# Kernel optimization log

Hardware: AMD Instinct MI355X
Metric: run time of the kernel (lower is better)

## Reference

```python
import jax, jax.numpy as jnp
import numpy as np

D_MODEL = 512
N_HEADS = 8
D_K = D_MODEL // N_HEADS


def setup_inputs() -> dict:
    key = jax.random.key(0)
    kq, kk, kv = jax.random.split(key, 3)
    shape = (4, 2048, D_MODEL)
    return {
        "Q": jax.random.normal(kq, shape, dtype=jnp.float32),
        "K": jax.random.normal(kk, shape, dtype=jnp.float32),
        "V": jax.random.normal(kv, shape, dtype=jnp.float32),
    }


def reference(Q, K, V):
    B, S, _ = Q.shape
    # [B, S, H, Dk] -> [B, H, S, Dk]
    q = Q.reshape(B, S, N_HEADS, D_K).transpose(0, 2, 1, 3)
    k = K.reshape(B, S, N_HEADS, D_K).transpose(0, 2, 1, 3)
    v = V.reshape(B, S, N_HEADS, D_K).transpose(0, 2, 1, 3)
    scale = 1.0 / (D_K ** 0.5)
    # [B, H, S, S] scores (faithful to original: full matrix materialized)
    scores = jnp.einsum("bhqd,bhkd->bhqk", q, k) * scale
    attn = jax.nn.softmax(scores, axis=-1)
    out = jnp.einsum("bhqk,bhkd->bhqd", attn, v)
    # [B, H, S, Dk] -> [B, S, D_MODEL]
    return out.transpose(0, 2, 1, 3).reshape(B, S, D_MODEL)
```

## Files before the change

kernel.cpp:

```cpp
#include <hip/hip_runtime.h>
#include <hip/hip_bf16.h>

#define SEQ    2048
#define DMODEL 512
#define NH     8
#define QBLK   128
#define KVB    64
#define NT     (SEQ / KVB)

#if __has_builtin(__builtin_amdgcn_exp2f)
#define EXPFN(x) __builtin_amdgcn_exp2f(x)
#define QSCALE 0.18033688011112042f
#else
#define EXPFN(x) __expf(x)
#define QSCALE 0.125f
#endif
#define THR 8.0f

typedef __attribute__((ext_vector_type(8)))  short bf16x8;
typedef __attribute__((ext_vector_type(16))) float f32x16;
typedef __attribute__((ext_vector_type(2)))  int   i32x2;

#define MFMA32(A, B, C) __builtin_amdgcn_mfma_f32_32x32x16_bf16(A, B, C, 0, 0, 0)

__device__ __forceinline__ unsigned short f2bf(float f) {
  union { float f; unsigned u; } x; x.f = f;
  return (unsigned short)((x.u + 0x7FFFu + ((x.u >> 16) & 1u)) >> 16);
}

__device__ __forceinline__ int cvtpk(float lo, float hi) {
  int r;
  asm("v_cvt_pk_bf16_f32 %0, %1, %2" : "=v"(r) : "v"(lo), "v"(hi));
  return r;
}

__device__ __forceinline__ i32x2 plswap(int a, int b) {
#if __has_builtin(__builtin_amdgcn_permlane32_swap)
  return __builtin_amdgcn_permlane32_swap(a, b, false, false);
#else
  int a2 = __shfl_xor(a, 32), b2 = __shfl_xor(b, 32);
  int hi = (threadIdx.x >> 5) & 1;
  i32x2 r; r.x = hi ? b2 : a; r.y = hi ? b : a2; return r;
#endif
}

__device__ __forceinline__ void gload16(const void* g, void* l) {
  __builtin_amdgcn_global_load_lds(
      (const __attribute__((address_space(1))) void*)g,
      (__attribute__((address_space(3))) void*)l, 16, 0, 0);
}


__global__ void prep_kv(const float* __restrict__ K, const float* __restrict__ V,
                        unsigned short* __restrict__ kb, unsigned short* __restrict__ vb) {
  if (blockIdx.x < 2048) {
    int gid = blockIdx.x * 256 + threadIdx.x;
    int g  = gid & 7;
    int s  = (gid >> 3) & (SEQ - 1);
    int bh = gid >> 14;
    int b = bh >> 3, h = bh & 7;
    const float* src = K + ((size_t)(b * SEQ + s) * DMODEL) + h * 64 + (g << 3);
    float4 a = ((const float4*)src)[0];
    float4 c = ((const float4*)src)[1];
    bf16x8 w;
    w[0] = (short)f2bf(a.x); w[1] = (short)f2bf(a.y);
    w[2] = (short)f2bf(a.z); w[3] = (short)f2bf(a.w);
    w[4] = (short)f2bf(c.x); w[5] = (short)f2bf(c.y);
    w[6] = (short)f2bf(c.z); w[7] = (short)f2bf(c.w);
    int r = s & 63;
    int slot = ((((r >> 5) << 3) + g) ^ (r & 15));
    unsigned short* dst = kb + ((size_t)bh * SEQ + (s & ~63)) * 64
                             + ((r & 31) << 7) + (slot << 3);
    *(bf16x8*)dst = w;
  } else {
    int bt = blockIdx.x - 2048;
    int bh = bt >> 5, tile = bt & 31;
    int b = bh >> 3, h = bh & 7;
    int t  = threadIdx.x;
    int d  = t & 63;
    int kg = t >> 6;
    const float* src = V + ((size_t)(b * SEQ + tile * 64 + kg * 16) * DMODEL) + h * 64 + d;
    float v[16];
#pragma unroll
    for (int j = 0; j < 16; ++j) v[j] = src[(size_t)j * DMODEL];
    bf16x8 lo, hi;
#pragma unroll
    for (int j = 0; j < 8; ++j) { lo[j] = (short)f2bf(v[j]); hi[j] = (short)f2bf(v[8 + j]); }
    unsigned short* base = vb + ((size_t)bt << 12);
    int g0 = kg << 1, g1 = (kg << 1) | 1;
    int rb = (((d >> 5) << 3));
    int s0 = ((rb + g0) ^ (d & 15));
    int s1 = ((rb + g1) ^ (d & 15));
    unsigned short* row = base + ((d & 31) << 7);
    *(bf16x8*)(row + (s0 << 3)) = lo;
    *(bf16x8*)(row + (s1 << 3)) = hi;
  }
}

__global__ __launch_bounds__(256, 2)
void fa_fwd(const float* __restrict__ Q, const unsigned short* __restrict__ Kb,
            const unsigned short* __restrict__ Vb, float* __restrict__ O) {
  __shared__ unsigned short kt[4][KVB * 64];
  __shared__ unsigned short vt[4][64 * KVB];

  const int tid = threadIdx.x;
  const int wv  = tid >> 6;
  const int ln  = tid & 63;
  const int l31 = ln & 31;
  const int hi  = ln >> 5;

  const int orig = blockIdx.x;
  const int wgid = (orig & 7) * 64 + (orig >> 3);
  const int bh = wgid >> 4;
  const int qt = wgid & 15;
  const int b = bh >> 3, h = bh & 7;

  const float* Qh = Q + (size_t)b * SEQ * DMODEL + (size_t)h * 64;
  float*       Oh = O + (size_t)b * SEQ * DMODEL + (size_t)h * 64;
  const unsigned short* Kh = Kb + (size_t)bh * SEQ * 64;
  const unsigned short* Vh = Vb + (size_t)bh * SEQ * 64;

  const int q = qt * QBLK + wv * 32 + l31;

  bf16x8 qf[4];
  {
    const float* qp = Qh + (size_t)q * DMODEL + (hi << 3);
#pragma unroll
    for (int t = 0; t < 4; ++t) {
      float4 a = *(const float4*)(qp + 16 * t);
      float4 c = *(const float4*)(qp + 16 * t + 4);
      bf16x8 w;
      w[0] = (short)f2bf(a.x * QSCALE); w[1] = (short)f2bf(a.y * QSCALE);
      w[2] = (short)f2bf(a.z * QSCALE); w[3] = (short)f2bf(a.w * QSCALE);
      w[4] = (short)f2bf(c.x * QSCALE); w[5] = (short)f2bf(c.y * QSCALE);
      w[6] = (short)f2bf(c.z * QSCALE); w[7] = (short)f2bf(c.w * QSCALE);
      qf[t] = w;
    }
  }

  const int rowb = l31 << 7;
  int ca[4], cb[4];
#pragma unroll
  for (int t = 0; t < 4; ++t) {
    int g = 2 * t + hi;
    ca[t] = rowb + (((g)     ^ (l31 & 15)) << 3);
    cb[t] = rowb + (((8 + g) ^ (l31 & 15)) << 3);
  }

  f32x16 o0 = {}, o1 = {};
  f32x16 sA0, sA1, sB0, sB1;
  float m = -__builtin_inff();
  float l = 0.f;

#define STAGE(T, B)                                                        \
  do {                                                                     \
    const char* gk = (const char*)(Kh + (size_t)(T) * KVB * 64);           \
    const char* gv = (const char*)(Vh + (size_t)(T) * KVB * 64);           \
    char* lk = (char*)&kt[(B)][0];                                         \
    char* lv = (char*)&vt[(B)][0];                                         \
    gload16(gk + (((wv)     * 64 + ln) << 4), lk + ((wv)     << 10));      \
    gload16(gk + (((wv + 4) * 64 + ln) << 4), lk + ((wv + 4) << 10));      \
    gload16(gv + (((wv)     * 64 + ln) << 4), lv + ((wv)     << 10));      \
    gload16(gv + (((wv + 4) * 64 + ln) << 4), lv + ((wv + 4) << 10));      \
  } while (0)

  auto qk = [&](const unsigned short* ktb, f32x16& t0, f32x16& t1) {
    f32x16 u0 = {}, u1 = {};
#pragma unroll
    for (int ks = 0; ks < 4; ++ks) {
      bf16x8 k0 = *(const bf16x8*)&ktb[ca[ks]];
      bf16x8 k1 = *(const bf16x8*)&ktb[cb[ks]];
      __builtin_amdgcn_s_setprio(1);
      u0 = MFMA32(k0, qf[ks], u0);
      u1 = MFMA32(k1, qf[ks], u1);
      __builtin_amdgcn_s_setprio(0);
    }
    t0 = u0; t1 = u1;
  };

  auto smpv = [&](f32x16& s0, f32x16& s1, const unsigned short* vtb) {
    float pm = fmaxf(s0[0], s0[1]);
#pragma unroll
    for (int j = 2; j < 16; ++j) pm = fmaxf(pm, s0[j]);
#pragma unroll
    for (int j = 0; j < 16; ++j) pm = fmaxf(pm, s1[j]);
    pm = fmaxf(pm, __shfl_xor(pm, 32));

    if (__any(pm > m + THR)) {
      float mn   = fmaxf(m, pm);
      float corr = EXPFN(m - mn);
      m = mn;
      l *= corr;
#pragma unroll
      for (int j = 0; j < 16; ++j) { o0[j] *= corr; o1[j] *= corr; }
    }

#pragma unroll
    for (int ks = 0; ks < 4; ++ks) {
      float e[8];
#pragma unroll
      for (int j = 0; j < 8; ++j) {
        float sv = (ks < 2) ? s0[(ks & 1) * 8 + j] : s1[(ks & 1) * 8 + j];
        e[j] = EXPFN(sv - m);
      }
      l += ((e[0] + e[1]) + (e[2] + e[3])) + ((e[4] + e[5]) + (e[6] + e[7]));
      i32x2 r0 = plswap(cvtpk(e[0], e[1]), cvtpk(e[4], e[5]));
      i32x2 r1 = plswap(cvtpk(e[2], e[3]), cvtpk(e[6], e[7]));
      union { int i[4]; bf16x8 v; } pa;
      pa.i[0] = r0.x; pa.i[1] = r1.x; pa.i[2] = r0.y; pa.i[3] = r1.y;

      bf16x8 v0 = *(const bf16x8*)&vtb[ca[ks]];
      bf16x8 v1 = *(const bf16x8*)&vtb[cb[ks]];
      __builtin_amdgcn_s_setprio(1);
      o0 = MFMA32(v0, pa.v, o0);
      o1 = MFMA32(v1, pa.v, o1);
      __builtin_amdgcn_s_setprio(0);
    }
  };

#define ITER(T, BC, BN, BS, SC0, SC1, SN0, SN1)                            \
  do {                                                                     \
    if ((T) + 2 < NT) STAGE((T) + 2, BS);                                  \
    if ((T) + 1 < NT) qk(kt[BN], SN0, SN1);                                \
    smpv(SC0, SC1, vt[BC]);                                                \
    __syncthreads();                                                       \
  } while (0)

  STAGE(0, 0);
  STAGE(1, 1);
  __syncthreads();
  qk(kt[0], sA0, sA1);

  for (int t = 0; t < NT; t += 4) {
    ITER(t + 0, 0, 1, 2, sA0, sA1, sB0, sB1);
    ITER(t + 1, 1, 2, 3, sB0, sB1, sA0, sA1);
    ITER(t + 2, 2, 3, 0, sA0, sA1, sB0, sB1);
    ITER(t + 3, 3, 0, 1, sB0, sB1, sA0, sA1);
  }

  l += __shfl_xor(l, 32);
  float rinv = 1.0f / l;
  float* op = Oh + (size_t)q * DMODEL;
#pragma unroll
  for (int r4 = 0; r4 < 4; ++r4) {
    float4 w0, w1;
    w0.x = o0[4 * r4 + 0] * rinv; w0.y = o0[4 * r4 + 1] * rinv;
    w0.z = o0[4 * r4 + 2] * rinv; w0.w = o0[4 * r4 + 3] * rinv;
    w1.x = o1[4 * r4 + 0] * rinv; w1.y = o1[4 * r4 + 1] * rinv;
    w1.z = o1[4 * r4 + 2] * rinv; w1.w = o1[4 * r4 + 3] * rinv;
    *(float4*)(op + 8 * r4 + 4 * hi)      = w0;
    *(float4*)(op + 32 + 8 * r4 + 4 * hi) = w1;
  }
}

extern "C" void kernel_launch(void* const* d_in, const int* in_sizes, int n_in,
                              void* d_out, int out_size, void* d_ws, size_t ws_size,
                              hipStream_t stream) {
  const float* Q = (const float*)d_in[0];
  const float* K = (const float*)d_in[1];
  const float* V = (const float*)d_in[2];
  float* O = (float*)d_out;
  unsigned short* kb = (unsigned short*)d_ws;
  unsigned short* vb = kb + (size_t)32 * SEQ * 64;
  prep_kv<<<3072, 256, 0, stream>>>(K, V, kb, vb);
  fa_fwd<<<512, 256, 0, stream>>>(Q, kb, vb, O);
}
```

Measured before the change: 63.30 us.

## Replace syncthreads with vmcnt-gated barriers and peel the pipelined KV loop

Swaps the full __syncthreads at the end of each iteration for a single s_waitcnt vmcnt(4) plus s_barrier placed after issuing the next stage's async loads. This lets the prefetch two tiles ahead stay in flight while the current tile is consumed. The last iterations are peeled so the in-loop bounds checks disappear. It also drops the s_setprio hints around the QK MFMAs and turns the row-max into a tree reduction to shorten the dependency chain. The risk is that barrier and waitcnt placement must correctly protect buffer reuse across the four LDS slots.

```diff
diff --git a/kernel.cpp b/kernel.cpp
--- a/kernel.cpp
+++ b/kernel.cpp
@@ -17,11 +17,14 @@
 #endif
 #define THR 8.0f
 
-typedef __attribute__((ext_vector_type(8)))  short bf16x8;
-typedef __attribute__((ext_vector_type(16))) float f32x16;
-typedef __attribute__((ext_vector_type(2)))  int   i32x2;
+typedef __attribute__((ext_vector_type(8)))  short     bf16x8;
+typedef __attribute__((ext_vector_type(16))) float     f32x16;
+typedef __attribute__((ext_vector_type(2)))  int       i32x2;
 
 #define MFMA32(A, B, C) __builtin_amdgcn_mfma_f32_32x32x16_bf16(A, B, C, 0, 0, 0)
+#define VMCNT(n) asm volatile("s_waitcnt vmcnt(" #n ")" ::: "memory")
+#define SBAR()   __builtin_amdgcn_s_barrier()
+#define SCHB()   __builtin_amdgcn_sched_barrier(0)
 
 __device__ __forceinline__ unsigned short f2bf(float f) {
   union { float f; unsigned u; } x; x.f = f;
@@ -49,7 +52,6 @@
       (const __attribute__((address_space(1))) void*)g,
       (__attribute__((address_space(3))) void*)l, 16, 0, 0);
 }
-
 
 __global__ void prep_kv(const float* __restrict__ K, const float* __restrict__ V,
                         unsigned short* __restrict__ kb, unsigned short* __restrict__ vb) {
@@ -170,21 +172,21 @@
     for (int ks = 0; ks < 4; ++ks) {
       bf16x8 k0 = *(const bf16x8*)&ktb[ca[ks]];
       bf16x8 k1 = *(const bf16x8*)&ktb[cb[ks]];
-      __builtin_amdgcn_s_setprio(1);
       u0 = MFMA32(k0, qf[ks], u0);
       u1 = MFMA32(k1, qf[ks], u1);
-      __builtin_amdgcn_s_setprio(0);
     }
     t0 = u0; t1 = u1;
   };
 
   auto smpv = [&](f32x16& s0, f32x16& s1, const unsigned short* vtb) {
-    float pm = fmaxf(s0[0], s0[1]);
-#pragma unroll
-    for (int j = 2; j < 16; ++j) pm = fmaxf(pm, s0[j]);
-#pragma unroll
-    for (int j = 0; j < 16; ++j) pm = fmaxf(pm, s1[j]);
-    pm = fmaxf(pm, __shfl_xor(pm, 32));
+    float mx[16];
+#pragma unroll
+    for (int j = 0; j < 16; ++j) mx[j] = fmaxf(s0[j], s1[j]);
+#pragma unroll
+    for (int w = 8; w > 0; w >>= 1)
+#pragma unroll
+      for (int j = 0; j < w; ++j) mx[j] = fmaxf(mx[j], mx[j + w]);
+    float pm = fmaxf(mx[0], __shfl_xor(mx[0], 32));
 
     if (__any(pm > m + THR)) {
       float mn   = fmaxf(m, pm);
@@ -218,25 +220,32 @@
     }
   };
 
-#define ITER(T, BC, BN, BS, SC0, SC1, SN0, SN1)                            \
+#define ITER(T, BS, BK, BV, SN0, SN1, SC0, SC1)                            \
   do {                                                                     \
-    if ((T) + 2 < NT) STAGE((T) + 2, BS);                                  \
-    if ((T) + 1 < NT) qk(kt[BN], SN0, SN1);                                \
-    smpv(SC0, SC1, vt[BC]);                                                \
-    __syncthreads();                                                       \
+    STAGE((T) + 2, BS);                                                    \
+    SCHB(); VMCNT(4); SBAR(); SCHB();                                      \
+    qk(kt[BK], SN0, SN1);                                                  \
+    smpv(SC0, SC1, vt[BV]);                                                \
   } while (0)
 
+  SCHB();
   STAGE(0, 0);
   STAGE(1, 1);
-  __syncthreads();
+  SCHB(); VMCNT(4); SBAR(); SCHB();
   qk(kt[0], sA0, sA1);
 
-  for (int t = 0; t < NT; t += 4) {
-    ITER(t + 0, 0, 1, 2, sA0, sA1, sB0, sB1);
-    ITER(t + 1, 1, 2, 3, sB0, sB1, sA0, sA1);
-    ITER(t + 2, 2, 3, 0, sA0, sA1, sB0, sB1);
-    ITER(t + 3, 3, 0, 1, sB0, sB1, sA0, sA1);
-  }
+  for (int t = 0; t < NT - 4; t += 4) {
+    ITER(t + 0, 2, 1, 0, sB0, sB1, sA0, sA1);
+    ITER(t + 1, 3, 2, 1, sA0, sA1, sB0, sB1);
+    ITER(t + 2, 0, 3, 2, sB0, sB1, sA0, sA1);
+    ITER(t + 3, 1, 0, 3, sA0, sA1, sB0, sB1);
+  }
+  ITER(28, 2, 1, 0, sB0, sB1, sA0, sA1);
+  ITER(29, 3, 2, 1, sA0, sA1, sB0, sB1);
+  SCHB(); VMCNT(0); SBAR(); SCHB();
+  qk(kt[3], sB0, sB1);
+  smpv(sA0, sA1, vt[2]);
+  smpv(sB0, sB1, vt[3]);
 
   l += __shfl_xor(l, 32);
   float rinv = 1.0f / l;
```

Result: no change. 64.14 us (+1.3%).
